# Performance work log

Measured on AMD Instinct MI355X. Metric: run time of the kernel, lower is better.

The kernel has to match this reference:

```python
import jax, jax.numpy as jnp
import numpy as np

DIM = 1024
HEADS = 16
DIM_HEAD = 64
INNER = HEADS * DIM_HEAD  # 1024
SCALE = DIM_HEAD ** (-0.5)
EPS = 1e-5


def _layernorm(x, g, b):
    mu = jnp.mean(x, axis=-1, keepdims=True)
    var = jnp.mean(jnp.square(x - mu), axis=-1, keepdims=True)
    return (x - mu) * jax.lax.rsqrt(var + EPS) * g + b


def _split_heads(t):
    # b t n (h d) -> b h t n d
    b, T, n, _ = t.shape
    return t.reshape(b, T, n, HEADS, DIM_HEAD).transpose(0, 3, 1, 2, 4)


def setup_inputs() -> dict:
    key = jax.random.key(0)
    ks = jax.random.split(key, 9)
    b, T, n1, n2 = 8, 4, 1024, 64
    x = jax.random.normal(ks[0], (b, T, n1, DIM), dtype=jnp.float32)
    latents = jax.random.normal(ks[1], (b, T, n2, DIM), dtype=jnp.float32)
    g_media = 1.0 + 0.02 * jax.random.normal(ks[2], (DIM,), dtype=jnp.float32)
    b_media = 0.02 * jax.random.normal(ks[3], (DIM,), dtype=jnp.float32)
    g_lat = 1.0 + 0.02 * jax.random.normal(ks[4], (DIM,), dtype=jnp.float32)
    b_lat = 0.02 * jax.random.normal(ks[5], (DIM,), dtype=jnp.float32)
    s = DIM ** (-0.5)
    Wq = jax.random.normal(ks[6], (DIM, INNER), dtype=jnp.float32) * s
    Wkv = jax.random.normal(ks[7], (DIM, 2 * INNER), dtype=jnp.float32) * s
    Wo = jax.random.normal(ks[8], (INNER, DIM), dtype=jnp.float32) * (INNER ** (-0.5))
    return {"x": x, "latents": latents, "g_media": g_media, "b_media": b_media,
            "g_lat": g_lat, "b_lat": b_lat, "Wq": Wq, "Wkv": Wkv, "Wo": Wo}


def reference(x, latents, g_media, b_media, g_lat, b_lat, Wq, Wkv, Wo):
    x = _layernorm(x, g_media, b_media)          # (b, T, n1, D)
    lat = _layernorm(latents, g_lat, b_lat)      # (b, T, n2, D)

    q = lat @ Wq                                 # (b, T, n2, inner)
    kv_input = jnp.concatenate((x, lat), axis=-2)  # (b, T, n1+n2, D)
    kv = kv_input @ Wkv                          # (b, T, n1+n2, 2*inner)
    k, v = jnp.split(kv, 2, axis=-1)

    q = _split_heads(q) * SCALE                  # (b, h, T, n2, d)
    k = _split_heads(k)                          # (b, h, T, n1+n2, d)
    v = _split_heads(v)

    sim = jnp.einsum('bhtid,bhtjd->bhtij', q, k)  # (b, h, T, n2, n1+n2)
    attn = jax.nn.softmax(sim, axis=-1)           # stable (amax subtracted)
    out = jnp.einsum('bhtij,bhtjd->bhtid', attn, v)

    # b h t n d -> b t n (h d)
    b, h, T, n, d = out.shape
    out = out.transpose(0, 2, 3, 1, 4).reshape(b, T, n, h * d)
    return out @ Wo
```

## Files before the change

### kernel.cpp

```cpp
#include <hip/hip_runtime.h>

#define DEVI __device__ __forceinline__

typedef unsigned short u16;
typedef unsigned int u32;

using bf16x8 = __attribute__((ext_vector_type(8))) short;
using f32x4  = __attribute__((ext_vector_type(4))) float;

DEVI u16 f2bf(float f) {
  u32 u = __builtin_bit_cast(u32, f);
  u32 r = (u + 0x7fffu + ((u >> 16) & 1u)) >> 16;
  return (u16)r;
}

DEVI void gl_lds16(const u16* g, u16* l) {
  __builtin_amdgcn_global_load_lds(
      (const __attribute__((address_space(1))) u32*)g,
      (__attribute__((address_space(3))) u32*)l, 16, 0, 0);
}

__global__ __launch_bounds__(256) void ln_kernel(
    const float* __restrict__ x, const float* __restrict__ lat,
    const float* __restrict__ gm, const float* __restrict__ bm,
    const float* __restrict__ gl, const float* __restrict__ bl,
    u16* __restrict__ kvin, u16* __restrict__ latb)
{
  int row = blockIdx.x;
  int bt = row / 1088, r = row % 1088;
  const float *src, *g, *b;
  bool is_lat = (r >= 1024);
  if (!is_lat) { src = x + ((size_t)bt*1024 + r)*1024; g = gm; b = bm; }
  else         { src = lat + ((size_t)bt*64 + (r-1024))*1024; g = gl; b = bl; }
  int tid = threadIdx.x;
  float4 v = *(const float4*)(src + tid*4);
  float s1 = v.x+v.y+v.z+v.w;
  float s2 = v.x*v.x+v.y*v.y+v.z*v.z+v.w*v.w;
  for (int off=32; off; off>>=1){ s1 += __shfl_down(s1,off); s2 += __shfl_down(s2,off); }
  __shared__ float red[2][4];
  int w = tid>>6, lane = tid&63;
  if (lane==0){ red[0][w]=s1; red[1][w]=s2; }
  __syncthreads();
  s1 = red[0][0]+red[0][1]+red[0][2]+red[0][3];
  s2 = red[1][0]+red[1][1]+red[1][2]+red[1][3];
  float mu = s1 * (1.f/1024.f);
  float var = s2 * (1.f/1024.f) - mu*mu;
  float rstd = rsqrtf(var + 1e-5f);
  float4 gv = *(const float4*)(g + tid*4);
  float4 bv = *(const float4*)(b + tid*4);
  ushort4 o;
  o.x = f2bf((v.x-mu)*rstd*gv.x + bv.x);
  o.y = f2bf((v.y-mu)*rstd*gv.y + bv.y);
  o.z = f2bf((v.z-mu)*rstd*gv.z + bv.z);
  o.w = f2bf((v.w-mu)*rstd*gv.w + bv.w);
  *(ushort4*)(kvin + (size_t)row*1024 + tid*4) = o;
  if (is_lat) *(ushort4*)(latb + ((size_t)(bt*64 + (r-1024)))*1024 + tid*4) = o;
}

__global__ __launch_bounds__(256) void transpose_cast(
    const float* __restrict__ in, u16* __restrict__ out, int R, int C)
{
  __shared__ float t[32][33];
  int bx = blockIdx.x*32, by = blockIdx.y*32;
  int tx = threadIdx.x & 31, ty = threadIdx.x >> 5;
  for (int k=0;k<32;k+=8) t[ty+k][tx] = in[(size_t)(by+ty+k)*C + bx+tx];
  __syncthreads();
  for (int k=0;k<32;k+=8) out[(size_t)(bx+ty+k)*R + by+tx] = f2bf(t[tx][ty+k]);
}

template<int MODE>
__global__ __launch_bounds__(256,2) void gemm_bt(
    const u16* __restrict__ A, const u16* __restrict__ BT,
    void* __restrict__ C0, void* __restrict__ C1,
    int M, int N, int K, float scale)
{
  __shared__ u16 lA[128*32];
  __shared__ u16 lB[128*32];
  int tid = threadIdx.x;
  int w = tid>>6, lane = tid&63;
  int li = lane&15, lg = lane>>4;
  int m0 = blockIdx.y*128, n0 = blockIdx.x*128;
  int wr = (w>>1)*64, wc = (w&1)*64;
  f32x4 acc[4][4] = {};
  int sr = lane>>2;
  int sk = ((lane&3) ^ ((lane>>3)&3))*8;
  const int rchunk = (lg ^ ((li>>1)&3))*8;
  const u16* pa = A  + (size_t)(m0 + w*32 + sr)*K + sk;
  const u16* pb = BT + (size_t)(n0 + w*32 + sr)*K + sk;
  u16* la0 = lA + (w*2)*512; u16* la1 = lA + (w*2+1)*512;
  u16* lb0 = lB + (w*2)*512; u16* lb1 = lB + (w*2+1)*512;
  for (int k0=0; k0<K; k0+=32) {
    gl_lds16(pa,        la0);
    gl_lds16(pa + 16*(size_t)K, la1);
    gl_lds16(pb,        lb0);
    gl_lds16(pb + 16*(size_t)K, lb1);
    pa += 32; pb += 32;
    __syncthreads();
    bf16x8 af[4], bfr[4];
    #pragma unroll
    for (int m=0;m<4;++m) af[m]  = *(const bf16x8*)(lA + (wr + m*16 + li)*32 + rchunk);
    #pragma unroll
    for (int n=0;n<4;++n) bfr[n] = *(const bf16x8*)(lB + (wc + n*16 + li)*32 + rchunk);
    #pragma unroll
    for (int m=0;m<4;++m)
      #pragma unroll
      for (int n=0;n<4;++n)
        acc[m][n] = __builtin_amdgcn_mfma_f32_16x16x32_bf16(af[m], bfr[n], acc[m][n], 0,0,0);
    __syncthreads();
  }
  if (MODE == 0) {
    u16* C = (u16*)C0;
    #pragma unroll
    for (int m=0;m<4;++m)
      #pragma unroll
      for (int n=0;n<4;++n) {
        int row = m0 + wr + m*16 + lg*4;
        int col = n0 + wc + n*16 + li;
        #pragma unroll
        for (int rg=0;rg<4;++rg)
          C[(size_t)(row+rg)*N + col] = f2bf(acc[m][n][rg]*scale);
      }
  } else {
    float* C = (float*)C0;
    #pragma unroll
    for (int m=0;m<4;++m)
      #pragma unroll
      for (int n=0;n<4;++n) {
        int row = m0 + wr + m*16 + lg*4;
        int col = n0 + wc + n*16 + li;
        #pragma unroll
        for (int rg=0;rg<4;++rg)
          C[(size_t)(row+rg)*N + col] = acc[m][n][rg]*scale;
      }
  }
}

__global__ __launch_bounds__(512,2) void gemm256_kv(
    const u16* __restrict__ A, const u16* __restrict__ BT,
    u16* __restrict__ kb, u16* __restrict__ vt)
{
  __shared__ u16 lds[2][2][2][256][32];
  const int tid = threadIdx.x;
  const int w = tid>>6, lane = tid&63;
  const int li = lane&15, lg = lane>>4;
  const int wm = w>>2, wn = w&3;
  const int bid = blockIdx.x;
  const int swz = (bid&7)*136 + (bid>>3);
  const int m0 = (swz>>3)*256, n0 = (swz&7)*256;
  const int srow = lane>>2;
  const int scol = ((lane&3) ^ ((lane>>3)&3))*8;
  const int rchunk = (lg ^ ((li>>1)&3))*8;

#define STAGE(b, mat, kh, kt) do {                                            \
    const u16* _s = (mat) ? BT : A;                                           \
    const int _base = (mat) ? n0 : m0;                                        \
    _Pragma("unroll")                                                         \
    for (int L=0; L<2; ++L) {                                                 \
      const int _r = L*128 + w*16;                                            \
      gl_lds16(_s + (size_t)(_base + _r + srow)*1024 + (kt)*64 + (kh)*32 + scol, \
               &lds[b][mat][kh][_r][0]);                                      \
    }                                                                         \
  } while(0)

  f32x4 acc[8][4] = {};

  STAGE(0,0,0,0); STAGE(0,1,0,0); STAGE(0,0,1,0); STAGE(0,1,1,0);
  asm volatile("s_waitcnt vmcnt(4)\n\ts_barrier" ::: "memory");

  for (int j=0; j<16; ++j) {
    const int c = j&1;
    const int ktn = (j<15) ? j+1 : 15;
    bf16x8 bfr[4];
    #pragma unroll
    for (int q=0; q<4; ++q) {
      const int kh = q>>1, mh = q&1;
      bf16x8 af[4];
      #pragma unroll
      for (int mf=0; mf<4; ++mf)
        af[mf] = *(const bf16x8*)&lds[c][0][kh][wm*128 + mh*64 + mf*16 + li][rchunk];
      if (mh==0) {
        #pragma unroll
        for (int nf=0; nf<4; ++nf)
          bfr[nf] = *(const bf16x8*)&lds[c][1][kh][wn*64 + nf*16 + li][rchunk];
      }
      if      (q==0) STAGE(c^1,0,0,ktn);
      else if (q==1) STAGE(c^1,1,0,ktn);
      else if (q==2) STAGE(c^1,0,1,ktn);
      else           STAGE(c^1,1,1,ktn);
      asm volatile("s_barrier" ::: "memory");
      __builtin_amdgcn_sched_barrier(0);
      __builtin_amdgcn_s_setprio(1);
      #pragma unroll
      for (int mf=0; mf<4; ++mf)
        #pragma unroll
        for (int nf=0; nf<4; ++nf)
          acc[mh*4+mf][nf] = __builtin_amdgcn_mfma_f32_16x16x32_bf16(af[mf], bfr[nf], acc[mh*4+mf][nf], 0,0,0);
      __builtin_amdgcn_s_setprio(0);
      if (q&1) asm volatile("s_waitcnt vmcnt(4)\n\ts_barrier" ::: "memory");
      else     asm volatile("s_barrier" ::: "memory");
    }
  }
#undef STAGE

  if (n0 < 1024) {
    #pragma unroll
    for (int am=0; am<8; ++am)
      #pragma unroll
      for (int nf=0; nf<4; ++nf) {
        int row = m0 + wm*128 + am*16 + lg*4;
        int col = n0 + wn*64 + nf*16 + li;
        #pragma unroll
        for (int rg=0; rg<4; ++rg)
          kb[(size_t)(row+rg)*1024 + col] = f2bf(acc[am][nf][rg]);
      }
  } else {
    #pragma unroll
    for (int am=0; am<8; ++am)
      #pragma unroll
      for (int nf=0; nf<4; ++nf) {
        int r0 = m0 + wm*128 + am*16 + lg*4;
        int cc = n0 + wn*64 + nf*16 + li - 1024;
        int bt = r0/1088, jj = r0 - bt*1088;
        ushort4 o;
        o.x = f2bf(acc[am][nf][0]); o.y = f2bf(acc[am][nf][1]);
        o.z = f2bf(acc[am][nf][2]); o.w = f2bf(acc[am][nf][3]);
        *(ushort4*)(vt + ((size_t)(bt*1024 + cc))*1088 + jj) = o;
      }
  }
}

__global__ __launch_bounds__(256,2) void attn_kernel(
    const u16* __restrict__ qbuf, const u16* __restrict__ kbuf,
    const u16* __restrict__ vT, u16* __restrict__ aout)
{
  __shared__ u16 p_im[4][16][72];
  int blk = blockIdx.x;
  int bt = blk >> 4, h = blk & 15;
  int w = threadIdx.x>>6, lane = threadIdx.x&63;
  int li = lane&15, lg = lane>>4;
  const u16* qrow = qbuf + ((size_t)(bt*64 + w*16 + li))*1024 + h*64;
  bf16x8 qf0 = *(const bf16x8*)(qrow + lg*8);
  bf16x8 qf1 = *(const bf16x8*)(qrow + 32 + lg*8);
  float mrun = -INFINITY, lrun = 0.f;
  f32x4 oacc[4] = {};
  const u16* kbase = kbuf + (size_t)bt*1088*1024 + h*64;
  const u16* vbase = vT + ((size_t)(bt*1024 + h*64))*1088;
  for (int c=0; c<17; ++c) {
    int j0 = c*64;
    f32x4 s[4] = {};
    #pragma unroll
    for (int jt=0; jt<4; ++jt) {
      const u16* krow = kbase + (size_t)(j0 + jt*16 + li)*1024;
      bf16x8 k0 = *(const bf16x8*)(krow + lg*8);
      bf16x8 k1 = *(const bf16x8*)(krow + 32 + lg*8);
      s[jt] = __builtin_amdgcn_mfma_f32_16x16x32_bf16(k0, qf0, s[jt], 0,0,0);
      s[jt] = __builtin_amdgcn_mfma_f32_16x16x32_bf16(k1, qf1, s[jt], 0,0,0);
    }
    float cm = -INFINITY;
    #pragma unroll
    for (int jt=0;jt<4;++jt)
      cm = fmaxf(cm, fmaxf(fmaxf(s[jt][0], s[jt][1]), fmaxf(s[jt][2], s[jt][3])));
    cm = fmaxf(cm, __shfl_xor(cm,16));
    cm = fmaxf(cm, __shfl_xor(cm,32));
    float mnew = fmaxf(mrun, cm);
    float sf = __expf(mrun - mnew);
    float ls = 0.f;
    #pragma unroll
    for (int jt=0;jt<4;++jt) {
      float p0 = __expf(s[jt][0]-mnew), p1 = __expf(s[jt][1]-mnew);
      float p2 = __expf(s[jt][2]-mnew), p3 = __expf(s[jt][3]-mnew);
      ls += p0+p1+p2+p3;
      ushort4 pk; pk.x = f2bf(p0); pk.y = f2bf(p1); pk.z = f2bf(p2); pk.w = f2bf(p3);
      *(ushort4*)&p_im[w][li][jt*16 + lg*4] = pk;
    }
    ls += __shfl_xor(ls,16);
    ls += __shfl_xor(ls,32);
    lrun = lrun*sf + ls;
    mrun = mnew;
    float sfr[4];
    #pragma unroll
    for (int rg=0;rg<4;++rg) sfr[rg] = __shfl(sf, lg*4+rg);
    #pragma unroll
    for (int dt=0;dt<4;++dt) {
      oacc[dt][0]*=sfr[0]; oacc[dt][1]*=sfr[1]; oacc[dt][2]*=sfr[2]; oacc[dt][3]*=sfr[3];
    }
    bf16x8 pa0 = *(const bf16x8*)&p_im[w][li][lg*8];
    bf16x8 pa1 = *(const bf16x8*)&p_im[w][li][32 + lg*8];
    #pragma unroll
    for (int dt=0;dt<4;++dt) {
      const u16* vrow = vbase + (size_t)(dt*16 + li)*1088 + j0;
      bf16x8 v0 = *(const bf16x8*)(vrow + lg*8);
      bf16x8 v1 = *(const bf16x8*)(vrow + 32 + lg*8);
      oacc[dt] = __builtin_amdgcn_mfma_f32_16x16x32_bf16(pa0, v0, oacc[dt], 0,0,0);
      oacc[dt] = __builtin_amdgcn_mfma_f32_16x16x32_bf16(pa1, v1, oacc[dt], 0,0,0);
    }
  }
  float linv[4];
  #pragma unroll
  for (int rg=0;rg<4;++rg) linv[rg] = 1.f / __shfl(lrun, lg*4+rg);
  u16* orow = aout + ((size_t)(bt*64 + w*16))*1024 + h*64;
  #pragma unroll
  for (int dt=0;dt<4;++dt)
    #pragma unroll
    for (int rg=0;rg<4;++rg)
      orow[(size_t)(lg*4+rg)*1024 + dt*16 + li] = f2bf(oacc[dt][rg]*linv[rg]);
}

extern "C" void kernel_launch(void* const* d_in, const int* in_sizes, int n_in,
                              void* d_out, int out_size, void* d_ws, size_t ws_size,
                              hipStream_t stream) {
  const float* x   = (const float*)d_in[0];
  const float* lat = (const float*)d_in[1];
  const float* gm  = (const float*)d_in[2];
  const float* bm  = (const float*)d_in[3];
  const float* gl  = (const float*)d_in[4];
  const float* bl  = (const float*)d_in[5];
  const float* Wq  = (const float*)d_in[6];
  const float* Wkv = (const float*)d_in[7];
  const float* Wo  = (const float*)d_in[8];
  float* out = (float*)d_out;

  char* ws = (char*)d_ws;
  const size_t KV_BYTES = (size_t)32*1088*1024*2;
  u16* kvin = (u16*)(ws);
  u16* kbuf = (u16*)(ws + KV_BYTES);
  u16* vT   = (u16*)(ws + 2*KV_BYTES);
  u16* latb = (u16*)(ws + 3*KV_BYTES);
  u16* qbuf = (u16*)(ws + 3*KV_BYTES + (size_t)4194304);
  u16* aout = (u16*)(ws + 3*KV_BYTES + (size_t)2*4194304);
  u16* wqT  = (u16*)(ws + 3*KV_BYTES + (size_t)3*4194304);
  u16* wkvT = (u16*)(ws + 3*KV_BYTES + (size_t)3*4194304 + 2097152);
  u16* woT  = (u16*)(ws + 3*KV_BYTES + (size_t)3*4194304 + 2097152 + 4194304);

  ln_kernel<<<dim3(32*1088), dim3(256), 0, stream>>>(x, lat, gm, bm, gl, bl, kvin, latb);
  transpose_cast<<<dim3(32,32), dim3(256), 0, stream>>>(Wq,  wqT,  1024, 1024);
  transpose_cast<<<dim3(64,32), dim3(256), 0, stream>>>(Wkv, wkvT, 1024, 2048);
  transpose_cast<<<dim3(32,32), dim3(256), 0, stream>>>(Wo,  woT,  1024, 1024);

  const float SCALE = 0.125f;
  gemm_bt<0><<<dim3(8,16),  dim3(256), 0, stream>>>(latb, wqT,  (void*)qbuf, nullptr, 2048, 1024, 1024, SCALE);
  gemm256_kv<<<dim3(1088), dim3(512), 0, stream>>>(kvin, wkvT, kbuf, vT);
  attn_kernel<<<dim3(512), dim3(256), 0, stream>>>(qbuf, kbuf, vT, aout);
  gemm_bt<1><<<dim3(8,16),  dim3(256), 0, stream>>>(aout, woT, (void*)out, nullptr, 2048, 1024, 1024, 1.f);
}
```

Before: 326.8 us.

## Fuse Q projection GEMM into KV GEMM launch and restructure k-loop pipeline

```diff
diff --git a/kernel.cpp b/kernel.cpp
--- a/kernel.cpp
+++ b/kernel.cpp
@@ -68,11 +68,9 @@
   for (int k=0;k<32;k+=8) out[(size_t)(bx+ty+k)*R + by+tx] = f2bf(t[tx][ty+k]);
 }
 
-template<int MODE>
-__global__ __launch_bounds__(256,2) void gemm_bt(
+__global__ __launch_bounds__(256,2) void gemm_bt_f32(
     const u16* __restrict__ A, const u16* __restrict__ BT,
-    void* __restrict__ C0, void* __restrict__ C1,
-    int M, int N, int K, float scale)
+    float* __restrict__ C, int N, int K)
 {
   __shared__ u16 lA[128*32];
   __shared__ u16 lB[128*32];
@@ -108,36 +106,22 @@
         acc[m][n] = __builtin_amdgcn_mfma_f32_16x16x32_bf16(af[m], bfr[n], acc[m][n], 0,0,0);
     __syncthreads();
   }
-  if (MODE == 0) {
-    u16* C = (u16*)C0;
-    #pragma unroll
-    for (int m=0;m<4;++m)
-      #pragma unroll
-      for (int n=0;n<4;++n) {
-        int row = m0 + wr + m*16 + lg*4;
-        int col = n0 + wc + n*16 + li;
-        #pragma unroll
-        for (int rg=0;rg<4;++rg)
-          C[(size_t)(row+rg)*N + col] = f2bf(acc[m][n][rg]*scale);
-      }
-  } else {
-    float* C = (float*)C0;
-    #pragma unroll
-    for (int m=0;m<4;++m)
-      #pragma unroll
-      for (int n=0;n<4;++n) {
-        int row = m0 + wr + m*16 + lg*4;
-        int col = n0 + wc + n*16 + li;
-        #pragma unroll
-        for (int rg=0;rg<4;++rg)
-          C[(size_t)(row+rg)*N + col] = acc[m][n][rg]*scale;
-      }
-  }
-}
-
-__global__ __launch_bounds__(512,2) void gemm256_kv(
+  #pragma unroll
+  for (int m=0;m<4;++m)
+    #pragma unroll
+    for (int n=0;n<4;++n) {
+      int row = m0 + wr + m*16 + lg*4;
+      int col = n0 + wc + n*16 + li;
+      #pragma unroll
+      for (int rg=0;rg<4;++rg)
+        C[(size_t)(row+rg)*N + col] = acc[m][n][rg];
+    }
+}
+
+__global__ __launch_bounds__(512,2) void gemm256_kvq(
     const u16* __restrict__ A, const u16* __restrict__ BT,
-    u16* __restrict__ kb, u16* __restrict__ vt)
+    const u16* __restrict__ Aq, const u16* __restrict__ BTq,
+    u16* __restrict__ kb, u16* __restrict__ vt, u16* __restrict__ qb)
 {
   __shared__ u16 lds[2][2][2][256][32];
   const int tid = threadIdx.x;
@@ -145,14 +129,17 @@
   const int li = lane&15, lg = lane>>4;
   const int wm = w>>2, wn = w&3;
   const int bid = blockIdx.x;
-  const int swz = (bid&7)*136 + (bid>>3);
-  const int m0 = (swz>>3)*256, n0 = (swz&7)*256;
+  const int swz = (bid&7)*140 + (bid>>3);
+  const bool is_q = (swz >= 1088);
+  const u16* Asrc; const u16* Bsrc; int m0, n0;
+  if (!is_q) { Asrc = A;  Bsrc = BT;  m0 = (swz>>3)*256;        n0 = (swz&7)*256; }
+  else       { int qt = swz-1088; Asrc = Aq; Bsrc = BTq; m0 = (qt>>2)*256; n0 = (qt&3)*256; }
   const int srow = lane>>2;
   const int scol = ((lane&3) ^ ((lane>>3)&3))*8;
   const int rchunk = (lg ^ ((li>>1)&3))*8;
 
 #define STAGE(b, mat, kh, kt) do {                                            \
-    const u16* _s = (mat) ? BT : A;                                           \
+    const u16* _s = (mat) ? Bsrc : Asrc;                                      \
     const int _base = (mat) ? n0 : m0;                                        \
     _Pragma("unroll")                                                         \
     for (int L=0; L<2; ++L) {                                                 \
@@ -165,44 +152,62 @@
   f32x4 acc[8][4] = {};
 
   STAGE(0,0,0,0); STAGE(0,1,0,0); STAGE(0,0,1,0); STAGE(0,1,1,0);
-  asm volatile("s_waitcnt vmcnt(4)\n\ts_barrier" ::: "memory");
+  asm volatile("s_waitcnt vmcnt(4) lgkmcnt(0)\n\ts_barrier" ::: "memory");
 
   for (int j=0; j<16; ++j) {
     const int c = j&1;
-    const int ktn = (j<15) ? j+1 : 15;
-    bf16x8 bfr[4];
-    #pragma unroll
-    for (int q=0; q<4; ++q) {
-      const int kh = q>>1, mh = q&1;
-      bf16x8 af[4];
-      #pragma unroll
-      for (int mf=0; mf<4; ++mf)
-        af[mf] = *(const bf16x8*)&lds[c][0][kh][wm*128 + mh*64 + mf*16 + li][rchunk];
-      if (mh==0) {
+    const int kt = (j<15) ? j+1 : 15;
+    STAGE(c^1,0,0,kt); STAGE(c^1,1,0,kt);
+    {
+      bf16x8 a0[8], b0[4];
+      #pragma unroll
+      for (int mf=0; mf<8; ++mf)
+        a0[mf] = *(const bf16x8*)&lds[c][0][0][wm*128 + mf*16 + li][rchunk];
+      #pragma unroll
+      for (int nf=0; nf<4; ++nf)
+        b0[nf] = *(const bf16x8*)&lds[c][1][0][wn*64 + nf*16 + li][rchunk];
+      __builtin_amdgcn_s_setprio(1);
+      #pragma unroll
+      for (int mf=0; mf<8; ++mf)
         #pragma unroll
         for (int nf=0; nf<4; ++nf)
-          bfr[nf] = *(const bf16x8*)&lds[c][1][kh][wn*64 + nf*16 + li][rchunk];
-      }
-      if      (q==0) STAGE(c^1,0,0,ktn);
-      else if (q==1) STAGE(c^1,1,0,ktn);
-      else if (q==2) STAGE(c^1,0,1,ktn);
-      else           STAGE(c^1,1,1,ktn);
-      asm volatile("s_barrier" ::: "memory");
-      __builtin_amdgcn_sched_barrier(0);
+          acc[mf][nf] = __builtin_amdgcn_mfma_f32_16x16x32_bf16(a0[mf], b0[nf], acc[mf][nf], 0,0,0);
+      __builtin_amdgcn_s_setprio(0);
+    }
+    asm volatile("s_waitcnt vmcnt(4) lgkmcnt(0)\n\ts_barrier" ::: "memory");
+    STAGE(c^1,0,1,kt); STAGE(c^1,1,1,kt);
+    {
+      bf16x8 a1[8], b1[4];
+      #pragma unroll
+      for (int mf=0; mf<8; ++mf)
+        a1[mf] = *(const bf16x8*)&lds[c][0][1][wm*128 + mf*16 + li][rchunk];
+      #pragma unroll
+      for (int nf=0; nf<4; ++nf)
+        b1[nf] = *(const bf16x8*)&lds[c][1][1][wn*64 + nf*16 + li][rchunk];
       __builtin_amdgcn_s_setprio(1);
       #pragma unroll
-      for (int mf=0; mf<4; ++mf)
+      for (int mf=0; mf<8; ++mf)
         #pragma unroll
         for (int nf=0; nf<4; ++nf)
-          acc[mh*4+mf][nf] = __builtin_amdgcn_mfma_f32_16x16x32_bf16(af[mf], bfr[nf], acc[mh*4+mf][nf], 0,0,0);
+          acc[mf][nf] = __builtin_amdgcn_mfma_f32_16x16x32_bf16(a1[mf], b1[nf], acc[mf][nf], 0,0,0);
       __builtin_amdgcn_s_setprio(0);
-      if (q&1) asm volatile("s_waitcnt vmcnt(4)\n\ts_barrier" ::: "memory");
-      else     asm volatile("s_barrier" ::: "memory");
-    }
+    }
+    asm volatile("s_waitcnt vmcnt(4) lgkmcnt(0)\n\ts_barrier" ::: "memory");
   }
 #undef STAGE
 
-  if (n0 < 1024) {
+  if (is_q) {
+    #pragma unroll
+    for (int am=0; am<8; ++am)
+      #pragma unroll
+      for (int nf=0; nf<4; ++nf) {
+        int row = m0 + wm*128 + am*16 + lg*4;
+        int col = n0 + wn*64 + nf*16 + li;
+        #pragma unroll
+        for (int rg=0; rg<4; ++rg)
+          qb[(size_t)(row+rg)*1024 + col] = f2bf(acc[am][nf][rg]*0.125f);
+      }
+  } else if (n0 < 1024) {
     #pragma unroll
     for (int am=0; am<8; ++am)
       #pragma unroll
@@ -337,9 +342,7 @@
   transpose_cast<<<dim3(64,32), dim3(256), 0, stream>>>(Wkv, wkvT, 1024, 2048);
   transpose_cast<<<dim3(32,32), dim3(256), 0, stream>>>(Wo,  woT,  1024, 1024);
 
-  const float SCALE = 0.125f;
-  gemm_bt<0><<<dim3(8,16),  dim3(256), 0, stream>>>(latb, wqT,  (void*)qbuf, nullptr, 2048, 1024, 1024, SCALE);
-  gemm256_kv<<<dim3(1088), dim3(512), 0, stream>>>(kvin, wkvT, kbuf, vT);
+  gemm256_kvq<<<dim3(1120), dim3(512), 0, stream>>>(kvin, wkvT, latb, wqT, kbuf, vT, qbuf);
   attn_kernel<<<dim3(512), dim3(256), 0, stream>>>(qbuf, kbuf, vT, aout);
-  gemm_bt<1><<<dim3(8,16),  dim3(256), 0, stream>>>(aout, woT, (void*)out, nullptr, 2048, 1024, 1024, 1.f);
-}
+  gemm_bt_f32<<<dim3(8,16), dim3(256), 0, stream>>>(aout, woT, out, 1024, 1024);
+}
```

Result: faster. 304.9 us (-6.7%).
